# Kernel tuning notes

Hardware: AMD Instinct MI355X
Metric: run time of the kernel (lower is better)

The kernel has to match this reference:

```python
import jax, jax.numpy as jnp
import numpy as np

KH = KW = 3   # kernel_size
PAD = 1       # padding on each side
B, C, H, W = 8, 3, 512, 512


def _unfold_operator(S, k, dtype=jnp.float32):
    # Block-diagonal identity pattern: op[a, c] = 1 iff a == c//k + c%k.
    # Shape [S, k*(S-k+1)]; matches Unfolder.create_right_operator.
    c = jnp.arange(k * (S - k + 1))
    rows = c // k + c % k
    return (jnp.arange(S)[:, None] == rows[None, :]).astype(dtype)


def setup_inputs() -> dict:
    key = jax.random.key(0)
    x = jax.random.normal(key, (B, C, H, W), dtype=jnp.float32)
    return {"x": x}


def reference(x) -> jnp.ndarray:
    # F.pad with (p,p,p,p) pads the last two dims
    xp = jnp.pad(x, ((0, 0), (0, 0), (PAD, PAD), (PAD, PAD)))
    Hs, Ws = xp.shape[-2], xp.shape[-1]
    # left operator: create_right_operator(size[::-1], kh).T -> [kh*(Hs-kh+1), Hs]
    L = _unfold_operator(Hs, KH, xp.dtype).T
    # right operator: [Ws, kw*(Ws-kw+1)]
    R = _unfold_operator(Ws, KW, xp.dtype)
    # out[b,c,p,q] = sum_{s,t} L[p,s] x[b,c,s,t] R[t,q]
    return jnp.einsum('ps,bcst,tq->bcpq', L, xp, R)
```

## Files before the change

### kernel.cpp

```cpp
#include <hip/hip_runtime.h>


#define B_N 8
#define C_N 3
#define H_N 512
#define W_N 512
#define HO 1536
#define WO 1536

__global__ __launch_bounds__(384) void unfold_rows_kernel(
    const float* __restrict__ x, float* __restrict__ out)
{
    const int p  = blockIdx.x;
    const int bc = blockIdx.y;

    const int s = p / 3 + p % 3 - 1;

    float4* orow = reinterpret_cast<float4*>(out + ((size_t)bc * HO + p) * WO);
    const int j = threadIdx.x;

    float4 v = make_float4(0.f, 0.f, 0.f, 0.f);
    if ((unsigned)s < (unsigned)H_N) {
        const float* __restrict__ xrow = x + ((size_t)bc * H_N + s) * W_N;
        const int q0 = j * 4;
        float vals[4];
#pragma unroll
        for (int e = 0; e < 4; ++e) {
            const int q = q0 + e;
            const int t = q / 3 + q % 3 - 1;
            vals[e] = ((unsigned)t < (unsigned)W_N) ? xrow[t] : 0.f;
        }
        v = make_float4(vals[0], vals[1], vals[2], vals[3]);
    }
    orow[j] = v;
}

extern "C" void kernel_launch(void* const* d_in, const int* in_sizes, int n_in,
                              void* d_out, int out_size, void* d_ws, size_t ws_size,
                              hipStream_t stream)
{
    const float* x = (const float*)d_in[0];
    float* out = (float*)d_out;

    dim3 grid(HO, B_N * C_N);
    dim3 block(WO / 4);
    unfold_rows_kernel<<<grid, block, 0, stream>>>(x, out);
}
```

Measured before the change: 49.37 us.

## Stage three input rows in LDS and emit three output rows per block

Each block now loads the three padded input rows it needs into shared memory with vectorized float4 loads. It then writes three consecutive output rows, each gathering from LDS. This replaces repeated scalar global gathers and cuts the grid by three. It adds a barrier and a larger per-block footprint, and the kernel stays bound by output writes.

```diff
diff --git a/kernel.cpp b/kernel.cpp
--- a/kernel.cpp
+++ b/kernel.cpp
@@ -8,31 +8,47 @@
 #define HO 1536
 #define WO 1536
 
-__global__ __launch_bounds__(384) void unfold_rows_kernel(
+__global__ __launch_bounds__(384) void unfold_lds_kernel(
     const float* __restrict__ x, float* __restrict__ out)
 {
-    const int p  = blockIdx.x;
+    const int a  = blockIdx.x;
     const int bc = blockIdx.y;
+    const int tid = threadIdx.x;
 
-    const int s = p / 3 + p % 3 - 1;
+    __shared__ float rows[3][W_N];
 
-    float4* orow = reinterpret_cast<float4*>(out + ((size_t)bc * HO + p) * WO);
-    const int j = threadIdx.x;
+    {
+        const int r  = tid >> 7;
+        const int cc = tid & 127;
+        const int s  = a - 1 + r;
+        float4 v = make_float4(0.f, 0.f, 0.f, 0.f);
+        if ((unsigned)s < (unsigned)H_N) {
+            v = reinterpret_cast<const float4*>(
+                    x + ((size_t)bc * H_N + s) * W_N)[cc];
+        }
+        reinterpret_cast<float4*>(&rows[r][0])[cc] = v;
+    }
+    __syncthreads();
 
-    float4 v = make_float4(0.f, 0.f, 0.f, 0.f);
-    if ((unsigned)s < (unsigned)H_N) {
-        const float* __restrict__ xrow = x + ((size_t)bc * H_N + s) * W_N;
-        const int q0 = j * 4;
+    int tcol[4];
+#pragma unroll
+    for (int e = 0; e < 4; ++e) {
+        const int q = tid * 4 + e;
+        tcol[e] = q / 3 + q % 3 - 1;
+    }
+
+    const size_t obase = ((size_t)bc * HO + 3 * (size_t)a) * WO;
+#pragma unroll
+    for (int d = 0; d < 3; ++d) {
         float vals[4];
 #pragma unroll
         for (int e = 0; e < 4; ++e) {
-            const int q = q0 + e;
-            const int t = q / 3 + q % 3 - 1;
-            vals[e] = ((unsigned)t < (unsigned)W_N) ? xrow[t] : 0.f;
+            const int t = tcol[e];
+            vals[e] = ((unsigned)t < (unsigned)W_N) ? rows[d][t] : 0.f;
         }
-        v = make_float4(vals[0], vals[1], vals[2], vals[3]);
+        reinterpret_cast<float4*>(out + obase + (size_t)d * WO)[tid] =
+            make_float4(vals[0], vals[1], vals[2], vals[3]);
     }
-    orow[j] = v;
 }
 
 extern "C" void kernel_launch(void* const* d_in, const int* in_sizes, int n_in,
@@ -42,7 +58,7 @@
     const float* x = (const float*)d_in[0];
     float* out = (float*)d_out;
 
-    dim3 grid(HO, B_N * C_N);
+    dim3 grid(H_N, B_N * C_N);
     dim3 block(WO / 4);
-    unfold_rows_kernel<<<grid, block, 0, stream>>>(x, out);
+    unfold_lds_kernel<<<grid, block, 0, stream>>>(x, out);
 }
```

New measurement: 48.71 us. No clear change (-1.3%).
